# Performance work log

Hardware: AMD Instinct MI355X
Metric: run time of the kernel (lower is better)

The kernel has to match this reference:

```python
import jax, jax.numpy as jnp
import numpy as np

B, C, D_IN, T = 8, 4, 256, 1024
D_MODEL = 256


def setup_inputs() -> dict:
    key = jax.random.key(0)
    k_x, k_m, k_wq, k_bq, k_wo, k_bo = jax.random.split(key, 6)
    x = jax.random.normal(k_x, (B, C, D_IN, T), dtype=jnp.float32)
    mask = jax.random.randint(k_m, (B, C, T, T), 0, 2) == 1  # bool, True = masked
    s_in = 1.0 / np.sqrt(D_IN)
    s_md = 1.0 / np.sqrt(D_MODEL)
    w_qkv = jax.random.uniform(k_wq, (3 * D_MODEL, D_IN), jnp.float32, -s_in, s_in)
    b_qkv = jax.random.uniform(k_bq, (3 * D_MODEL,), jnp.float32, -s_in, s_in)
    w_out = jax.random.uniform(k_wo, (D_MODEL, D_MODEL), jnp.float32, -s_md, s_md)
    b_out = jax.random.uniform(k_bo, (D_MODEL,), jnp.float32, -s_md, s_md)
    return {"x": x, "mask": mask, "w_qkv": w_qkv, "b_qkv": b_qkv,
            "w_out": w_out, "b_out": b_out}


def reference(x, mask, w_qkv, b_qkv, w_out, b_out):
    # x: (B, C, d_in, t) -> (B, C, t, d_in)
    xt = jnp.swapaxes(x, -1, -2)
    qkv = jnp.einsum('bctd,ed->bcte', xt, w_qkv) + b_qkv  # (B,C,t,3*d_model)
    q, k, v = jnp.split(qkv, 3, axis=-1)
    scale = 1.0 / jnp.sqrt(jnp.asarray(q.shape[-1], dtype=q.dtype))
    scores = jnp.einsum('bcqd,bckd->bcqk', q, k) * scale  # (B,C,t,t)
    scores = jnp.where(mask, -jnp.inf, scores)
    attn = jax.nn.softmax(scores, axis=-1)
    out = jnp.einsum('bcqk,bckd->bcqd', attn, v)          # (B,C,t,d_model)
    return jnp.einsum('bcqd,ed->bcqe', out, w_out) + b_out
```

## Files before the change

### kernel.cpp

```cpp
#include <hip/hip_runtime.h>
#include <hip/hip_bf16.h>

#define TT 1024
#define DM 256
#define BCN 32

typedef __attribute__((ext_vector_type(8))) short short8;
typedef __attribute__((ext_vector_type(4))) short short4v;
typedef __attribute__((ext_vector_type(4))) float f32x4;

__device__ __forceinline__ void wg_barrier_lds() {
  asm volatile("s_waitcnt lgkmcnt(0)\n\ts_barrier" ::: "memory");
}

__device__ __forceinline__ short bf16b(float f) {
  __hip_bfloat16 h = __float2bfloat16(f);
  return *(short*)&h;
}

__device__ __forceinline__ void dma16(void* l, const void* g) {
  __builtin_amdgcn_global_load_lds(
      (const __attribute__((address_space(1))) void*)g,
      (__attribute__((address_space(3))) void*)l, 16, 0, 0);
}
__device__ __forceinline__ void dma4(void* l, const void* g) {
  __builtin_amdgcn_global_load_lds(
      (const __attribute__((address_space(1))) void*)g,
      (__attribute__((address_space(3))) void*)l, 4, 0, 0);
}

__global__ __launch_bounds__(256) void prep_kernel(
    const float* __restrict__ w_qkv, const float* __restrict__ w_out,
    __hip_bfloat16* __restrict__ Wb, __hip_bfloat16* __restrict__ Wo)
{
  int idx = blockIdx.x * 256 + threadIdx.x;
  const float* src;
  __hip_bfloat16* dst;
  if (idx < 24576) { src = w_qkv; dst = Wb; }
  else { idx -= 24576; src = w_out; dst = Wo; }
  const int r = idx >> 5, ch = idx & 31;
  const float4* wv4 = (const float4*)src + (size_t)r * 64 + ch * 2;
  const float4 f0 = wv4[0], f1 = wv4[1];
  short8 pk;
  pk[0] = bf16b(f0.x); pk[1] = bf16b(f0.y);
  pk[2] = bf16b(f0.z); pk[3] = bf16b(f0.w);
  pk[4] = bf16b(f1.x); pk[5] = bf16b(f1.y);
  pk[6] = bf16b(f1.z); pk[7] = bf16b(f1.w);
  *(short8*)&dst[(size_t)r * 256 + ((ch ^ (r & 7)) << 3)] = pk;
}

__global__ __launch_bounds__(256, 8) void mask_kernel(
    const int* __restrict__ mask, unsigned* __restrict__ mbits)
{
  const int tid = threadIdx.x;
  __shared__ unsigned Wlds[64][33];
  const int m = blockIdx.x;
  const int bc = m >> 4, q0 = (m & 15) * 64;
  const int w = tid >> 6, l = tid & 63;
  const int4* base =
      (const int4*)(mask + (size_t)(bc * 1024 + q0 + w * 16) * 1024) + l;
  int4 v[4], n[4];
#pragma unroll
  for (int s = 0; s < 4; ++s) v[s] = base[s * 64];
#pragma unroll 1
  for (int rr = 0; rr < 16; ++rr) {
    if (rr < 15) {
      const int4* nb = base + (rr + 1) * 256;
#pragma unroll
      for (int s = 0; s < 4; ++s) n[s] = nb[s * 64];
    }
    const int ql = w * 16 + rr;
#pragma unroll
    for (int s = 0; s < 4; ++s) {
      const unsigned long long bx = __ballot(v[s].x != 0);
      const unsigned long long by = __ballot(v[s].y != 0);
      const unsigned long long bz = __ballot(v[s].z != 0);
      const unsigned long long bw = __ballot(v[s].w != 0);
      if (l < 8) {
        const unsigned word =
            (unsigned)((bx >> (8 * l)) & 0xFF) |
            ((unsigned)((by >> (8 * l)) & 0xFF) << 8) |
            ((unsigned)((bz >> (8 * l)) & 0xFF) << 16) |
            ((unsigned)((bw >> (8 * l)) & 0xFF) << 24);
        Wlds[ql][s * 8 + l] = word;
      }
    }
#pragma unroll
    for (int s = 0; s < 4; ++s) v[s] = n[s];
  }
  __syncthreads();
  unsigned* mb = mbits + (size_t)bc * 32 * 1024 + q0;
#pragma unroll
  for (int i = 0; i < 8; ++i) {
    const int idx = tid + i * 256, j = idx >> 6, ql = idx & 63;
    mb[(size_t)j * 1024 + ql] = Wlds[ql][j];
  }
}

__global__ __launch_bounds__(256, 2) void qkv_kernel(
    const float* __restrict__ x, const __hip_bfloat16* __restrict__ Wb,
    const float* __restrict__ b_qkv,
    __hip_bfloat16* __restrict__ Qb, __hip_bfloat16* __restrict__ Kb,
    __hip_bfloat16* __restrict__ Vtb)
{
  const int tid = threadIdx.x;

  __shared__ __attribute__((aligned(16))) __hip_bfloat16 Xs[64][264];
  __shared__ __attribute__((aligned(16))) __hip_bfloat16 Wd[2][32 * 256];
  __shared__ __attribute__((aligned(16))) float bls[768];

  const int tt = blockIdx.x & 15, bc = blockIdx.x >> 4;
  const int t0 = tt * 64;
  const int w = tid >> 6, l = tid & 63, quad = l >> 4, lm = l & 15;
  const int lm7 = lm & 7;

  const char* Wg = (const char*)Wb;
  auto wissue = [&](int it, int buf) {
    const char* g = Wg + (size_t)it * 16384 + w * 4096 + l * 16;
    char* d = (char*)&Wd[buf][0] + w * 4096;
#pragma unroll
    for (int i = 0; i < 4; ++i) dma16(d + i * 1024, g + i * 1024);
  };

  wissue(0, 0);
  wissue(1, 1);

  if (tid < 192) {
    const float4 bv = *(const float4*)(b_qkv + tid * 4);
    *(float4*)&bls[tid * 4] = bv;
  }

  {
    const float* xbc = x + (size_t)bc * DM * TT;
    const int t4 = (tid & 15) * 4;
    for (int s = 0; s < 4; ++s) {
      const int d4 = (tid >> 4) * 4 + s * 64;
      f32x4 f[4];
#pragma unroll
      for (int r = 0; r < 4; ++r)
        f[r] = *(const f32x4*)(xbc + (size_t)(d4 + r) * TT + t0 + t4);
#pragma unroll
      for (int r = 0; r < 4; ++r) {
        short4v pk;
#pragma unroll
        for (int c = 0; c < 4; ++c) pk[c] = bf16b(f[c][r]);
        *(short4v*)&Xs[t4 + r][d4] = pk;
      }
    }
  }

#pragma unroll 1
  for (int it = 0; it < 24; ++it) {
    const int buf = it & 1;
    if (it == 0)
      asm volatile("s_waitcnt vmcnt(4)" ::: "memory");
    else if (it < 23)
      asm volatile("s_waitcnt vmcnt(6)" ::: "memory");
    else
      asm volatile("s_waitcnt vmcnt(2)" ::: "memory");
    wg_barrier_lds();

    const int e0 = it * 32;
    const bool vmode = (it >= 16);
    const __hip_bfloat16* WT = &Wd[buf][0];
    f32x4 acc[2] = {};
#pragma unroll
    for (int ks = 0; ks < 8; ++ks) {
      const int k = ks * 32 + quad * 8;
      const short8 xa = *(const short8*)&Xs[w * 16 + lm][k];
      const int c = ((ks * 4 + quad) ^ lm7) << 3;
#pragma unroll
      for (int nt = 0; nt < 2; ++nt) {
        const short8 wb2 = *(const short8*)&WT[(nt * 16 + lm) * 256 + c];
        acc[nt] = vmode
            ? __builtin_amdgcn_mfma_f32_16x16x32_bf16(xa, wb2, acc[nt], 0, 0, 0)
            : __builtin_amdgcn_mfma_f32_16x16x32_bf16(wb2, xa, acc[nt], 0, 0, 0);
      }
    }

    if (it < 8) {
      const int t = t0 + w * 16 + lm;
#pragma unroll
      for (int nt = 0; nt < 2; ++nt) {
        const int ebase = e0 + nt * 16 + quad * 4;
        const f32x4 bb = *(const f32x4*)&bls[ebase];
        short4v pk;
#pragma unroll
        for (int r = 0; r < 4; ++r) pk[r] = bf16b(acc[nt][r] + bb[r]);
        *(short4v*)&Qb[((size_t)bc * TT + t) * DM + ebase] = pk;
      }
    } else if (!vmode) {
      const int t = t0 + w * 16 + lm;
#pragma unroll
      for (int nt = 0; nt < 2; ++nt) {
        const int eg = e0 + nt * 16 + quad * 4;
        const int eK = eg - 256;
        const f32x4 bb = *(const f32x4*)&bls[eg];
        short4v pk;
#pragma unroll
        for (int r = 0; r < 4; ++r) pk[r] = bf16b(acc[nt][r] + bb[r]);
        const int ch = eK >> 3;
        const int off = (((ch ^ (t & 7)) << 3) | (eK & 7));
        *(short4v*)&Kb[((size_t)bc * TT + t) * DM + off] = pk;
      }
    } else {
      const int tb = w * 16 + quad * 4;
      const int kb = tt * 2 + (tb >> 5), tloc = tb & 31;
#pragma unroll
      for (int nt = 0; nt < 2; ++nt) {
        const int e = (e0 - 512) + nt * 16 + lm;
        const float bq = bls[512 + e];
        short4v pk;
#pragma unroll
        for (int r = 0; r < 4; ++r) pk[r] = bf16b(acc[nt][r] + bq);
        *(short4v*)&Vtb[(((size_t)bc * 32 + kb) * 256 + e) * 32 + tloc] = pk;
      }
    }

    wg_barrier_lds();
    if (it < 22) wissue(it + 2, buf);
  }
}

__global__ __launch_bounds__(256, 2) void attn_kernel(
    const __hip_bfloat16* __restrict__ Qb, const __hip_bfloat16* __restrict__ Kb,
    const __hip_bfloat16* __restrict__ Vtb, const unsigned* __restrict__ Mbits,
    const __hip_bfloat16* __restrict__ Wob, const float* __restrict__ b_out,
    float* __restrict__ out)
{
  const int fid = blockIdx.x;
  const int xcd = fid & 7, slot = fid >> 3;
  const int bc = xcd * 4 + (slot >> 4);
  const int qt = slot & 15;
  const int q0 = qt * 64;

  __shared__ __attribute__((aligned(16))) char smem[72192];
  __hip_bfloat16* Ks = (__hip_bfloat16*)smem;
  __hip_bfloat16* Vs = (__hip_bfloat16*)(smem + 32768);
  __hip_bfloat16 (*Ps)[40] = (__hip_bfloat16(*)[40])(smem + 65536);
  unsigned* Msb = (unsigned*)(smem + 70656);
  float* bout = (float*)(smem + 71168);
  __hip_bfloat16 (*Os)[264] = (__hip_bfloat16(*)[264])smem;
  __hip_bfloat16* Wo = (__hip_bfloat16*)(smem + 33792);

  const int tid = threadIdx.x, w = tid >> 6, l = tid & 63;
  const int quad = l >> 4, lm = l & 15, lm7 = lm & 7;
  const int trow = w * 16 + lm;

  if (tid < 64) {
    const f32x4 bv = *(const f32x4*)(b_out + tid * 4);
    *(f32x4*)&bout[tid * 4] = bv;
  }

  const __hip_bfloat16* Qg =
      Qb + ((size_t)bc * TT + q0 + trow) * DM + quad * 8;
  short8 qf[8];
#pragma unroll
  for (int ks = 0; ks < 8; ++ks) qf[ks] = *(const short8*)(Qg + ks * 32);

  const char* KgT = (const char*)(Kb + (size_t)bc * TT * DM);
  const char* VgT = (const char*)(Vtb + (size_t)bc * TT * DM);
  const unsigned* MgT = Mbits + ((size_t)bc * 32) * 1024 + q0;

  short8 ones;
#pragma unroll
  for (int i = 0; i < 8; ++i) ones[i] = (short)0x3F80;

  f32x4 Oa[16] = {};
  f32x4 Ol = {};

  auto issue = [&](int j, int buf) {
    const char* kg = KgT + (size_t)j * 16384 + w * 4096 + l * 16;
    const char* vg = VgT + (size_t)j * 16384 + w * 4096 + l * 16;
    char* kl = (char*)Ks + buf * 16384 + w * 4096;
    char* vl = (char*)Vs + buf * 16384 + w * 4096;
#pragma unroll
    for (int i = 0; i < 4; ++i) dma16(kl + i * 1024, kg + i * 1024);
#pragma unroll
    for (int i = 0; i < 4; ++i) dma16(vl + i * 1024, vg + i * 1024);
    dma4((char*)Msb + buf * 256, MgT + (size_t)j * 1024 + l);
  };

  auto compute = [&](int buf) {
    const __hip_bfloat16* KT = Ks + buf * 8192;
    const __hip_bfloat16* VT = Vs + buf * 8192;
    f32x4 Sa0 = {}, Sa1 = {};
#pragma unroll
    for (int ks = 0; ks < 8; ++ks) {
      const int c = ((ks * 4 + quad) ^ lm7) << 3;
      const short8 a0 = *(const short8*)&KT[lm * 256 + c];
      const short8 a1 = *(const short8*)&KT[(lm + 16) * 256 + c];
      Sa0 = __builtin_amdgcn_mfma_f32_16x16x32_bf16(a0, qf[ks], Sa0, 0, 0, 0);
      Sa1 = __builtin_amdgcn_mfma_f32_16x16x32_bf16(a1, qf[ks], Sa1, 0, 0, 0);
    }
    const unsigned mw = Msb[buf * 64 + trow];
#pragma unroll
    for (int nt = 0; nt < 2; ++nt) {
      const f32x4 Sa = nt ? Sa1 : Sa0;
      short4v pk;
#pragma unroll
      for (int r = 0; r < 4; ++r) {
        const float p = ((mw >> (nt * 4 + quad + 8 * r)) & 1u)
                            ? 0.f
                            : __expf(fmaf(Sa[r], 0.0625f, -8.0f));
        pk[r] = bf16b(p);
      }
      *(short4v*)&Ps[trow][nt * 16 + quad * 4] = pk;
    }
    const short8 pf = *(const short8*)&Ps[trow][quad * 8];
#pragma unroll
    for (int ct = 0; ct < 16; ++ct) {
      const short8 a = *(const short8*)&VT[(ct * 16 + lm) * 32 + quad * 8];
      Oa[ct] = __builtin_amdgcn_mfma_f32_16x16x32_bf16(a, pf, Oa[ct], 0, 0, 0);
    }
    Ol = __builtin_amdgcn_mfma_f32_16x16x32_bf16(ones, pf, Ol, 0, 0, 0);
  };

  issue(0, 0);
  issue(1, 1);
#pragma unroll 1
  for (int j = 0; j < 32; ++j) {
    const int buf = j & 1;
    if (j < 31)
      asm volatile("s_waitcnt vmcnt(9)" ::: "memory");
    else
      asm volatile("s_waitcnt vmcnt(0)" ::: "memory");
    asm volatile("s_barrier" ::: "memory");
    compute(buf);
    wg_barrier_lds();
    if (j < 30) issue(j + 2, buf);
  }

  const float inv = 1.0f / Ol[0];
#pragma unroll
  for (int ct = 0; ct < 16; ++ct) {
    short4v pk;
#pragma unroll
    for (int r = 0; r < 4; ++r) pk[r] = bf16b(Oa[ct][r] * inv);
    *(short4v*)&Os[trow][ct * 16 + quad * 4] = pk;
  }
  wg_barrier_lds();

  short8 osr[8];
#pragma unroll
  for (int ks = 0; ks < 8; ++ks)
    osr[ks] = *(const short8*)&Os[trow][ks * 32 + quad * 8];

  const char* WoG = (const char*)Wob;
  auto pissue = [&](int it, int buf) {
    const char* g = WoG + (size_t)it * 16384 + w * 4096 + l * 16;
    char* d = (char*)Wo + buf * 16384 + w * 4096;
#pragma unroll
    for (int i = 0; i < 4; ++i) dma16(d + i * 1024, g + i * 1024);
  };
  pissue(0, 0);
  pissue(1, 1);

  float* outp = out + ((size_t)bc * TT + q0 + trow) * DM;
#pragma unroll 1
  for (int it = 0; it < 8; ++it) {
    const int buf = it & 1;
    if (it == 0)
      asm volatile("s_waitcnt vmcnt(4)" ::: "memory");
    else if (it < 7)
      asm volatile("s_waitcnt vmcnt(6)" ::: "memory");
    else
      asm volatile("s_waitcnt vmcnt(2)" ::: "memory");
    wg_barrier_lds();

    f32x4 acc[2] = {};
#pragma unroll
    for (int ks = 0; ks < 8; ++ks) {
      const int c = ((ks * 4 + quad) ^ lm7) << 3;
#pragma unroll
      for (int nt = 0; nt < 2; ++nt) {
        const short8 wa = *(const short8*)&Wo[buf * 8192 + (nt * 16 + lm) * 256 + c];
        acc[nt] = __builtin_amdgcn_mfma_f32_16x16x32_bf16(wa, osr[ks], acc[nt], 0, 0, 0);
      }
    }
#pragma unroll
    for (int nt = 0; nt < 2; ++nt) {
      const int fb = it * 32 + nt * 16 + quad * 4;
      const f32x4 bb = *(const f32x4*)&bout[fb];
      float4 o;
      o.x = acc[nt][0] + bb[0];
      o.y = acc[nt][1] + bb[1];
      o.z = acc[nt][2] + bb[2];
      o.w = acc[nt][3] + bb[3];
      *(float4*)&outp[fb] = o;
    }

    wg_barrier_lds();
    if (it < 6) pissue(it + 2, buf);
  }
}

extern "C" void kernel_launch(void* const* d_in, const int* in_sizes, int n_in,
                              void* d_out, int out_size, void* d_ws, size_t ws_size,
                              hipStream_t stream) {
  const float* x = (const float*)d_in[0];
  const int* mask = (const int*)d_in[1];
  const float* w_qkv = (const float*)d_in[2];
  const float* b_qkv = (const float*)d_in[3];
  const float* w_out = (const float*)d_in[4];
  const float* b_out = (const float*)d_in[5];
  float* out = (float*)d_out;

  const size_t N = (size_t)BCN * TT * DM;
  __hip_bfloat16* Qb  = (__hip_bfloat16*)d_ws;
  __hip_bfloat16* Kb  = Qb + N;
  __hip_bfloat16* Vtb = Kb + N;
  unsigned* Mbits     = (unsigned*)(Vtb + N);
  __hip_bfloat16* Wbp = (__hip_bfloat16*)(Mbits + (size_t)BCN * 32 * 1024);
  __hip_bfloat16* Wob = Wbp + 768 * 256;

  prep_kernel<<<dim3(128), dim3(256), 0, stream>>>(w_qkv, w_out, Wbp, Wob);
  mask_kernel<<<dim3(512), dim3(256), 0, stream>>>(mask, Mbits);
  qkv_kernel<<<dim3(512), dim3(256), 0, stream>>>(x, Wbp, b_qkv, Qb, Kb, Vtb);
  attn_kernel<<<dim3(512), dim3(256), 0, stream>>>(Qb, Kb, Vtb, Mbits,
                                                   Wob, b_out, out);
}
```

Measured before the change: 324.7 us.

## Fuse all four kernels into one cooperative persistent kernel with grid syncs

Replaces the four separate launches (weight prep, mask bit-packing, QKV projection, attention plus output projection) with a single cooperative kernel of 512 blocks. Grid-wide barriers separate the phases, and LDS is reused across them through one shared byte buffer. The goal is to remove launch gaps and per-kernel tail effects. In exchange, every block must stay resident, since 512 blocks at 2 per CU need 256 CUs, and two grid.sync barriers are added. If the cooperative launch fails, the code falls back to the original four launches.

```diff
diff --git a/kernel.cpp b/kernel.cpp
--- a/kernel.cpp
+++ b/kernel.cpp
@@ -1,5 +1,8 @@
 #include <hip/hip_runtime.h>
 #include <hip/hip_bf16.h>
+#include <hip/hip_cooperative_groups.h>
+
+namespace cg = cooperative_groups;
 
 #define TT 1024
 #define DM 256
@@ -27,6 +30,372 @@
   __builtin_amdgcn_global_load_lds(
       (const __attribute__((address_space(1))) void*)g,
       (__attribute__((address_space(3))) void*)l, 4, 0, 0);
+}
+
+__global__ __launch_bounds__(256, 2) void mega_kernel(
+    const float* __restrict__ x, const int* __restrict__ maskp,
+    const float* __restrict__ w_qkv, const float* __restrict__ b_qkv,
+    const float* __restrict__ w_out, const float* __restrict__ b_out,
+    __hip_bfloat16* __restrict__ Qb, __hip_bfloat16* __restrict__ Kb,
+    __hip_bfloat16* __restrict__ Vtb, unsigned* __restrict__ mbits,
+    __hip_bfloat16* __restrict__ Wb, __hip_bfloat16* __restrict__ Wog,
+    float* __restrict__ out)
+{
+  cg::grid_group grid = cg::this_grid();
+  __shared__ __attribute__((aligned(16))) char smem[72192];
+
+  const int tid = threadIdx.x, b = blockIdx.x;
+  const int w = tid >> 6, l = tid & 63;
+  const int quad = l >> 4, lm = l & 15, lm7 = lm & 7;
+  const int trow = w * 16 + lm;
+
+  if (tid < 64) {
+    int idx = b * 64 + tid;
+    const float* src;
+    __hip_bfloat16* dst;
+    if (idx < 24576) { src = w_qkv; dst = Wb; }
+    else { idx -= 24576; src = w_out; dst = Wog; }
+    const int r = idx >> 5, ch = idx & 31;
+    const float4* wv4 = (const float4*)src + (size_t)r * 64 + ch * 2;
+    const float4 f0 = wv4[0], f1 = wv4[1];
+    short8 pk;
+    pk[0] = bf16b(f0.x); pk[1] = bf16b(f0.y);
+    pk[2] = bf16b(f0.z); pk[3] = bf16b(f0.w);
+    pk[4] = bf16b(f1.x); pk[5] = bf16b(f1.y);
+    pk[6] = bf16b(f1.z); pk[7] = bf16b(f1.w);
+    *(short8*)&dst[(size_t)r * 256 + ((ch ^ (r & 7)) << 3)] = pk;
+  }
+
+  {
+    unsigned (*Wlds)[33] = (unsigned(*)[33])smem;
+    const int bc = b >> 4, q0 = (b & 15) * 64;
+    const int4* base =
+        (const int4*)(maskp + (size_t)(bc * 1024 + q0 + w * 16) * 1024) + l;
+    int4 v[4], n[4];
+#pragma unroll
+    for (int s = 0; s < 4; ++s) v[s] = base[s * 64];
+#pragma unroll 1
+    for (int rr = 0; rr < 16; ++rr) {
+      if (rr < 15) {
+        const int4* nb = base + (rr + 1) * 256;
+#pragma unroll
+        for (int s = 0; s < 4; ++s) n[s] = nb[s * 64];
+      }
+      const int ql = w * 16 + rr;
+#pragma unroll
+      for (int s = 0; s < 4; ++s) {
+        const unsigned long long bx = __ballot(v[s].x != 0);
+        const unsigned long long by = __ballot(v[s].y != 0);
+        const unsigned long long bz = __ballot(v[s].z != 0);
+        const unsigned long long bw = __ballot(v[s].w != 0);
+        if (l < 8) {
+          const unsigned word =
+              (unsigned)((bx >> (8 * l)) & 0xFF) |
+              ((unsigned)((by >> (8 * l)) & 0xFF) << 8) |
+              ((unsigned)((bz >> (8 * l)) & 0xFF) << 16) |
+              ((unsigned)((bw >> (8 * l)) & 0xFF) << 24);
+          Wlds[ql][s * 8 + l] = word;
+        }
+      }
+#pragma unroll
+      for (int s = 0; s < 4; ++s) v[s] = n[s];
+    }
+    __syncthreads();
+    unsigned* mb = mbits + (size_t)bc * 32 * 1024 + q0;
+#pragma unroll
+    for (int i = 0; i < 8; ++i) {
+      const int idx = tid + i * 256, j = idx >> 6, ql = idx & 63;
+      mb[(size_t)j * 1024 + ql] = Wlds[ql][j];
+    }
+  }
+
+  asm volatile("s_waitcnt vmcnt(0) lgkmcnt(0)" ::: "memory");
+  __threadfence();
+  grid.sync();
+
+  {
+    __hip_bfloat16 (*Xs)[264] = (__hip_bfloat16(*)[264])smem;
+    __hip_bfloat16* Wd = (__hip_bfloat16*)(smem + 33792);
+    float* bls = (float*)(smem + 66560);
+
+    const int tt = b & 15, bc = b >> 4;
+    const int t0 = tt * 64;
+
+    const char* Wg = (const char*)Wb;
+    auto wissue = [&](int it, int buf) {
+      const char* g = Wg + (size_t)it * 16384 + w * 4096 + l * 16;
+      char* d = (char*)Wd + buf * 16384 + w * 4096;
+#pragma unroll
+      for (int i = 0; i < 4; ++i) dma16(d + i * 1024, g + i * 1024);
+    };
+
+    wissue(0, 0);
+    wissue(1, 1);
+
+    if (tid < 192) {
+      const float4 bv = *(const float4*)(b_qkv + tid * 4);
+      *(float4*)&bls[tid * 4] = bv;
+    }
+
+    {
+      const float* xbc = x + (size_t)bc * DM * TT;
+      const int t4 = (tid & 15) * 4;
+      for (int s = 0; s < 4; ++s) {
+        const int d4 = (tid >> 4) * 4 + s * 64;
+        f32x4 f[4];
+#pragma unroll
+        for (int r = 0; r < 4; ++r)
+          f[r] = *(const f32x4*)(xbc + (size_t)(d4 + r) * TT + t0 + t4);
+#pragma unroll
+        for (int r = 0; r < 4; ++r) {
+          short4v pk;
+#pragma unroll
+          for (int c = 0; c < 4; ++c) pk[c] = bf16b(f[c][r]);
+          *(short4v*)&Xs[t4 + r][d4] = pk;
+        }
+      }
+    }
+
+#pragma unroll 1
+    for (int it = 0; it < 24; ++it) {
+      const int buf = it & 1;
+      if (it == 0)
+        asm volatile("s_waitcnt vmcnt(4)" ::: "memory");
+      else if (it < 23)
+        asm volatile("s_waitcnt vmcnt(6)" ::: "memory");
+      else
+        asm volatile("s_waitcnt vmcnt(2)" ::: "memory");
+      wg_barrier_lds();
+
+      const int e0 = it * 32;
+      const bool vmode = (it >= 16);
+      const __hip_bfloat16* WT = Wd + buf * 8192;
+      f32x4 acc[2] = {};
+#pragma unroll
+      for (int ks = 0; ks < 8; ++ks) {
+        const int k = ks * 32 + quad * 8;
+        const short8 xa = *(const short8*)&Xs[trow][k];
+        const int c = ((ks * 4 + quad) ^ lm7) << 3;
+#pragma unroll
+        for (int nt = 0; nt < 2; ++nt) {
+          const short8 wb2 = *(const short8*)&WT[(nt * 16 + lm) * 256 + c];
+          acc[nt] = vmode
+              ? __builtin_amdgcn_mfma_f32_16x16x32_bf16(xa, wb2, acc[nt], 0, 0, 0)
+              : __builtin_amdgcn_mfma_f32_16x16x32_bf16(wb2, xa, acc[nt], 0, 0, 0);
+        }
+      }
+
+      if (it < 8) {
+        const int t = t0 + trow;
+#pragma unroll
+        for (int nt = 0; nt < 2; ++nt) {
+          const int ebase = e0 + nt * 16 + quad * 4;
+          const f32x4 bb = *(const f32x4*)&bls[ebase];
+          short4v pk;
+#pragma unroll
+          for (int r = 0; r < 4; ++r) pk[r] = bf16b(acc[nt][r] + bb[r]);
+          *(short4v*)&Qb[((size_t)bc * TT + t) * DM + ebase] = pk;
+        }
+      } else if (!vmode) {
+        const int t = t0 + trow;
+#pragma unroll
+        for (int nt = 0; nt < 2; ++nt) {
+          const int eg = e0 + nt * 16 + quad * 4;
+          const int eK = eg - 256;
+          const f32x4 bb = *(const f32x4*)&bls[eg];
+          short4v pk;
+#pragma unroll
+          for (int r = 0; r < 4; ++r) pk[r] = bf16b(acc[nt][r] + bb[r]);
+          const int ch = eK >> 3;
+          const int off = (((ch ^ (t & 7)) << 3) | (eK & 7));
+          *(short4v*)&Kb[((size_t)bc * TT + t) * DM + off] = pk;
+        }
+      } else {
+        const int tb = w * 16 + quad * 4;
+        const int kb = tt * 2 + (tb >> 5), tloc = tb & 31;
+#pragma unroll
+        for (int nt = 0; nt < 2; ++nt) {
+          const int e = (e0 - 512) + nt * 16 + lm;
+          const float bq = bls[512 + e];
+          short4v pk;
+#pragma unroll
+          for (int r = 0; r < 4; ++r) pk[r] = bf16b(acc[nt][r] + bq);
+          *(short4v*)&Vtb[(((size_t)bc * 32 + kb) * 256 + e) * 32 + tloc] = pk;
+        }
+      }
+
+      wg_barrier_lds();
+      if (it < 22) wissue(it + 2, buf);
+    }
+  }
+
+  asm volatile("s_waitcnt vmcnt(0) lgkmcnt(0)" ::: "memory");
+  __threadfence();
+  grid.sync();
+
+  {
+    const int xcd = b & 7, slot = b >> 3;
+    const int bc = xcd * 4 + (slot >> 4);
+    const int qt = slot & 15;
+    const int q0 = qt * 64;
+
+    __hip_bfloat16* Ks = (__hip_bfloat16*)smem;
+    __hip_bfloat16* Vs = (__hip_bfloat16*)(smem + 32768);
+    __hip_bfloat16 (*Ps)[40] = (__hip_bfloat16(*)[40])(smem + 65536);
+    unsigned* Msb = (unsigned*)(smem + 70656);
+    float* bout = (float*)(smem + 71168);
+    __hip_bfloat16 (*Os)[264] = (__hip_bfloat16(*)[264])smem;
+    __hip_bfloat16* Wo = (__hip_bfloat16*)(smem + 33792);
+
+    if (tid < 64) {
+      const f32x4 bv = *(const f32x4*)(b_out + tid * 4);
+      *(f32x4*)&bout[tid * 4] = bv;
+    }
+
+    const __hip_bfloat16* Qg =
+        Qb + ((size_t)bc * TT + q0 + trow) * DM + quad * 8;
+    short8 qf[8];
+#pragma unroll
+    for (int ks = 0; ks < 8; ++ks) qf[ks] = *(const short8*)(Qg + ks * 32);
+
+    const char* KgT = (const char*)(Kb + (size_t)bc * TT * DM);
+    const char* VgT = (const char*)(Vtb + (size_t)bc * TT * DM);
+    const unsigned* MgT = mbits + ((size_t)bc * 32) * 1024 + q0;
+
+    short8 ones;
+#pragma unroll
+    for (int i = 0; i < 8; ++i) ones[i] = (short)0x3F80;
+
+    f32x4 Oa[16] = {};
+    f32x4 Ol = {};
+
+    auto issue = [&](int j, int buf) {
+      const char* kg = KgT + (size_t)j * 16384 + w * 4096 + l * 16;
+      const char* vg = VgT + (size_t)j * 16384 + w * 4096 + l * 16;
+      char* kl = (char*)Ks + buf * 16384 + w * 4096;
+      char* vl = (char*)Vs + buf * 16384 + w * 4096;
+#pragma unroll
+      for (int i = 0; i < 4; ++i) dma16(kl + i * 1024, kg + i * 1024);
+#pragma unroll
+      for (int i = 0; i < 4; ++i) dma16(vl + i * 1024, vg + i * 1024);
+      dma4((char*)Msb + buf * 256, MgT + (size_t)j * 1024 + l);
+    };
+
+    auto compute = [&](int buf) {
+      const __hip_bfloat16* KT = Ks + buf * 8192;
+      const __hip_bfloat16* VT = Vs + buf * 8192;
+      f32x4 Sa0 = {}, Sa1 = {};
+#pragma unroll
+      for (int ks = 0; ks < 8; ++ks) {
+        const int c = ((ks * 4 + quad) ^ lm7) << 3;
+        const short8 a0 = *(const short8*)&KT[lm * 256 + c];
+        const short8 a1 = *(const short8*)&KT[(lm + 16) * 256 + c];
+        Sa0 = __builtin_amdgcn_mfma_f32_16x16x32_bf16(a0, qf[ks], Sa0, 0, 0, 0);
+        Sa1 = __builtin_amdgcn_mfma_f32_16x16x32_bf16(a1, qf[ks], Sa1, 0, 0, 0);
+      }
+      const unsigned mw = Msb[buf * 64 + trow];
+#pragma unroll
+      for (int nt = 0; nt < 2; ++nt) {
+        const f32x4 Sa = nt ? Sa1 : Sa0;
+        short4v pk;
+#pragma unroll
+        for (int r = 0; r < 4; ++r) {
+          const float p = ((mw >> (nt * 4 + quad + 8 * r)) & 1u)
+                              ? 0.f
+                              : __expf(fmaf(Sa[r], 0.0625f, -8.0f));
+          pk[r] = bf16b(p);
+        }
+        *(short4v*)&Ps[trow][nt * 16 + quad * 4] = pk;
+      }
+      const short8 pf = *(const short8*)&Ps[trow][quad * 8];
+#pragma unroll
+      for (int ct = 0; ct < 16; ++ct) {
+        const short8 a = *(const short8*)&VT[(ct * 16 + lm) * 32 + quad * 8];
+        Oa[ct] = __builtin_amdgcn_mfma_f32_16x16x32_bf16(a, pf, Oa[ct], 0, 0, 0);
+      }
+      Ol = __builtin_amdgcn_mfma_f32_16x16x32_bf16(ones, pf, Ol, 0, 0, 0);
+    };
+
+    issue(0, 0);
+    issue(1, 1);
+#pragma unroll 1
+    for (int j = 0; j < 32; ++j) {
+      const int buf = j & 1;
+      if (j < 31)
+        asm volatile("s_waitcnt vmcnt(9)" ::: "memory");
+      else
+        asm volatile("s_waitcnt vmcnt(0)" ::: "memory");
+      asm volatile("s_barrier" ::: "memory");
+      compute(buf);
+      wg_barrier_lds();
+      if (j < 30) issue(j + 2, buf);
+    }
+
+    const float inv = 1.0f / Ol[0];
+#pragma unroll
+    for (int ct = 0; ct < 16; ++ct) {
+      short4v pk;
+#pragma unroll
+      for (int r = 0; r < 4; ++r) pk[r] = bf16b(Oa[ct][r] * inv);
+      *(short4v*)&Os[trow][ct * 16 + quad * 4] = pk;
+    }
+    wg_barrier_lds();
+
+    short8 osr[8];
+#pragma unroll
+    for (int ks = 0; ks < 8; ++ks)
+      osr[ks] = *(const short8*)&Os[trow][ks * 32 + quad * 8];
+
+    const char* WoG = (const char*)Wog;
+    auto pissue = [&](int it, int buf) {
+      const char* g = WoG + (size_t)it * 16384 + w * 4096 + l * 16;
+      char* d = (char*)Wo + buf * 16384 + w * 4096;
+#pragma unroll
+      for (int i = 0; i < 4; ++i) dma16(d + i * 1024, g + i * 1024);
+    };
+    pissue(0, 0);
+    pissue(1, 1);
+
+    float* outp = out + ((size_t)bc * TT + q0 + trow) * DM;
+#pragma unroll 1
+    for (int it = 0; it < 8; ++it) {
+      const int buf = it & 1;
+      if (it == 0)
+        asm volatile("s_waitcnt vmcnt(4)" ::: "memory");
+      else if (it < 7)
+        asm volatile("s_waitcnt vmcnt(6)" ::: "memory");
+      else
+        asm volatile("s_waitcnt vmcnt(2)" ::: "memory");
+      wg_barrier_lds();
+
+      f32x4 acc[2] = {};
+#pragma unroll
+      for (int ks = 0; ks < 8; ++ks) {
+        const int c = ((ks * 4 + quad) ^ lm7) << 3;
+#pragma unroll
+        for (int nt = 0; nt < 2; ++nt) {
+          const short8 wa =
+              *(const short8*)&Wo[buf * 8192 + (nt * 16 + lm) * 256 + c];
+          acc[nt] =
+              __builtin_amdgcn_mfma_f32_16x16x32_bf16(wa, osr[ks], acc[nt], 0, 0, 0);
+        }
+      }
+#pragma unroll
+      for (int nt = 0; nt < 2; ++nt) {
+        const int fb = it * 32 + nt * 16 + quad * 4;
+        const f32x4 bb = *(const f32x4*)&bout[fb];
+        float4 o;
+        o.x = acc[nt][0] + bb[0];
+        o.y = acc[nt][1] + bb[1];
+        o.z = acc[nt][2] + bb[2];
+        o.w = acc[nt][3] + bb[3];
+        *(float4*)&outp[fb] = o;
+      }
+
+      wg_barrier_lds();
+      if (it < 6) pissue(it + 2, buf);
+    }
+  }
 }
 
 __global__ __launch_bounds__(256) void prep_kernel(
@@ -104,7 +473,6 @@
     __hip_bfloat16* __restrict__ Vtb)
 {
   const int tid = threadIdx.x;
-
   __shared__ __attribute__((aligned(16))) __hip_bfloat16 Xs[64][264];
   __shared__ __attribute__((aligned(16))) __hip_bfloat16 Wd[2][32 * 256];
   __shared__ __attribute__((aligned(16))) float bls[768];
@@ -414,9 +782,17 @@
   __hip_bfloat16* Wbp = (__hip_bfloat16*)(Mbits + (size_t)BCN * 32 * 1024);
   __hip_bfloat16* Wob = Wbp + 768 * 256;
 
-  prep_kernel<<<dim3(128), dim3(256), 0, stream>>>(w_qkv, w_out, Wbp, Wob);
-  mask_kernel<<<dim3(512), dim3(256), 0, stream>>>(mask, Mbits);
-  qkv_kernel<<<dim3(512), dim3(256), 0, stream>>>(x, Wbp, b_qkv, Qb, Kb, Vtb);
-  attn_kernel<<<dim3(512), dim3(256), 0, stream>>>(Qb, Kb, Vtb, Mbits,
-                                                   Wob, b_out, out);
-}
+  void* kargs[] = {(void*)&x,     (void*)&mask,  (void*)&w_qkv, (void*)&b_qkv,
+                   (void*)&w_out, (void*)&b_out, (void*)&Qb,    (void*)&Kb,
+                   (void*)&Vtb,   (void*)&Mbits, (void*)&Wbp,   (void*)&Wob,
+                   (void*)&out};
+  hipError_t err = hipLaunchCooperativeKernel(
+      (const void*)mega_kernel, dim3(512), dim3(256), kargs, 0, stream);
+  if (err != hipSuccess) {
+    prep_kernel<<<dim3(128), dim3(256), 0, stream>>>(w_qkv, w_out, Wbp, Wob);
+    mask_kernel<<<dim3(512), dim3(256), 0, stream>>>(mask, Mbits);
+    qkv_kernel<<<dim3(512), dim3(256), 0, stream>>>(x, Wbp, b_qkv, Qb, Kb, Vtb);
+    attn_kernel<<<dim3(512), dim3(256), 0, stream>>>(Qb, Kb, Vtb, Mbits,
+                                                     Wob, b_out, out);
+  }
+}
```

Measured after the change: 550.1 us. 69.4% more time.
